# Kernel optimization log

Measured on AMD Instinct MI355X. Metric: run time of the kernel, lower is better.

The kernel has to match this reference:

```python
import jax, jax.numpy as jnp
import numpy as np

B, S = 65536, 128          # batch of tasks, support set size
MAX_CLASSES = 10
STATS_DIM = MAX_CLASSES + 4  # hist + [n_nonzero, entropy, subset_size, hist_max]
TOKEN_DIM = 256


def setup_inputs() -> dict:
    key = jax.random.key(0)
    k1, k2, k3, k4, k5 = jax.random.split(key, 5)
    y_support = jax.random.randint(k1, (B, S), 0, MAX_CLASSES, dtype=jnp.int32)
    # MLP params: Linear(14, D) -> GELU -> Linear(D, D)
    w1 = jax.random.normal(k2, (STATS_DIM, TOKEN_DIM), jnp.float32) / np.sqrt(STATS_DIM)
    b1 = jax.random.normal(k3, (TOKEN_DIM,), jnp.float32) * 0.01
    w2 = jax.random.normal(k4, (TOKEN_DIM, TOKEN_DIM), jnp.float32) / np.sqrt(TOKEN_DIM)
    b2 = jax.random.normal(k5, (TOKEN_DIM,), jnp.float32) * 0.01
    return {"y_support": y_support, "w1": w1, "b1": b1, "w2": w2, "b2": b2}


def reference(y_support, w1, b1, w2, b2):
    b, s = y_support.shape
    # Batched bincount via scatter-add: hist[i, c] = #{j : y_support[i, j] == c}
    rows = jnp.arange(b, dtype=jnp.int32)[:, None]              # [B, 1]
    hist = jnp.zeros((b, MAX_CLASSES), jnp.float32).at[rows, y_support].add(1.0)
    total = jnp.maximum(hist.sum(axis=-1, keepdims=True), 1.0)  # clamp_min(1.0)
    p = hist / total                                            # [B, C]
    entropy = -(p * jnp.log(p + 1e-6)).sum(axis=-1)             # [B]
    n_nonzero = (p > 0).sum(axis=-1).astype(jnp.float32)        # [B]
    stats = jnp.concatenate([
        p,
        n_nonzero[:, None],
        entropy[:, None],
        jnp.full((b, 1), float(s), jnp.float32),
        p.max(axis=-1, keepdims=True),
    ], axis=1)                                                  # [B, C+4]
    h = jax.nn.gelu(stats @ w1 + b1, approximate=False)         # exact GELU like nn.GELU
    return h @ w2 + b2                                          # [B, TOKEN_DIM]
```

## Files before the change

### kernel.cpp

```cpp
#include <hip/hip_runtime.h>
#include <stdint.h>


#define SSUP 128
#define DD   256

typedef __attribute__((ext_vector_type(8)))  short bf16x8;
typedef __attribute__((ext_vector_type(16))) float f32x16;

__device__ __forceinline__ unsigned f2bf_u(float f) {
    union { float f; unsigned u; } v; v.f = f;
    return (v.u + 0x7FFFu + ((v.u >> 16) & 1u)) >> 16;
}
__device__ __forceinline__ unsigned pk2(float a, float b) {
    return f2bf_u(a) | (f2bf_u(b) << 16);
}

__device__ __forceinline__ float gelu_f(float x) {
    float z = 0.7978845608028654f * x * (1.0f + 0.044715f * x * x);
    float e = __expf(-2.0f * z);
    float th = 2.0f / (1.0f + e) - 1.0f;
    return 0.5f * x * (1.0f + th);
}

__global__ void prep_kernel(const float* __restrict__ w1,
                            const float* __restrict__ w2,
                            unsigned short* __restrict__ w1f,
                            unsigned short* __restrict__ w2f) {
    int tid = blockIdx.x * 256 + threadIdx.x;
    if (tid < 8192) {
        int l  = tid & 63;
        int nt = (tid >> 6) & 7;
        int s  = tid >> 9;
        int n  = nt * 32 + (l & 31);
        int k0 = s * 16 + (l >> 5) * 8;
        unsigned pk[4];
        #pragma unroll
        for (int h = 0; h < 4; ++h)
            pk[h] = pk2(w2[(size_t)(k0 + 2*h) * DD + n],
                        w2[(size_t)(k0 + 2*h + 1) * DD + n]);
        *(uint4*)&w2f[(size_t)tid * 8] = make_uint4(pk[0], pk[1], pk[2], pk[3]);
    } else if (tid < 8704) {
        int idx = tid - 8192;
        int l   = idx & 63;
        int nt  = idx >> 6;
        int n   = nt * 32 + (l & 31);
        int kk0 = (l >> 5) * 8;
        unsigned pk[4];
        #pragma unroll
        for (int h = 0; h < 4; ++h) {
            int ka = kk0 + 2*h, kb = kk0 + 2*h + 1;
            float fa = (ka < 14) ? w1[(size_t)ka * DD + n] : 0.0f;
            float fb = (kb < 14) ? w1[(size_t)kb * DD + n] : 0.0f;
            pk[h] = pk2(fa, fb);
        }
        *(uint4*)&w1f[(size_t)idx * 8] = make_uint4(pk[0], pk[1], pk[2], pk[3]);
    }
}

__global__ __launch_bounds__(256, 4)
void encoder_kernel(const int* __restrict__ y,
                    const float* __restrict__ b1,
                    const float* __restrict__ b2,
                    const unsigned short* __restrict__ w1f,
                    const unsigned short* __restrict__ w2f,
                    float* __restrict__ out) {
    __shared__ __align__(16) unsigned short stats_a[64][16];
    __shared__ __align__(16) unsigned short h_lds[64][264];

    const int tid = threadIdx.x;
    const int r0 = blockIdx.x * 64;

    const int rl = tid >> 2;
    const int q  = tid & 3;
    const int4* yp = (const int4*)(y + (size_t)(r0 + rl) * SSUP);
    unsigned long long pkc = 0ull;
    #pragma unroll
    for (int i = 0; i < 8; ++i) {
        int4 v = yp[i * 4 + q];
        pkc += 1ull << (6 * v.x);
        pkc += 1ull << (6 * v.y);
        pkc += 1ull << (6 * v.z);
        pkc += 1ull << (6 * v.w);
    }
    float p[10]; float ent = 0.f, pmax = 0.f, nnz = 0.f;
    #pragma unroll
    for (int c = 0; c < 10; ++c) {
        int cc = (int)((pkc >> (6 * c)) & 63ull);
        cc += __shfl_xor(cc, 1);
        cc += __shfl_xor(cc, 2);
        float pc = (float)cc * 0.0078125f;
        p[c] = pc;
        nnz += (cc > 0) ? 1.0f : 0.0f;
        ent -= pc * __logf(pc + 1e-6f);
        pmax = fmaxf(pmax, pc);
    }
    if (q < 2) {
        unsigned a0, a1, a2, a3;
        if (q == 0) { a0 = pk2(p[0], p[1]); a1 = pk2(p[2], p[3]);
                      a2 = pk2(p[4], p[5]); a3 = pk2(p[6], p[7]); }
        else        { a0 = pk2(p[8], p[9]); a1 = pk2(nnz, ent);
                      a2 = pk2(128.0f, pmax); a3 = 0u; }
        *(uint4*)&stats_a[rl][q * 8] = make_uint4(a0, a1, a2, a3);
    }
    __syncthreads();

    const int lane = tid & 63;
    const int wid  = tid >> 6;
    const int wm   = wid & 1;
    const int wn   = wid >> 1;
    const int l31  = lane & 31;
    const int lh   = lane >> 5;

    bf16x8 af1 = *(const bf16x8*)&stats_a[32 * wm + l31][lh * 8];
    #pragma unroll
    for (int t = 0; t < 4; ++t) {
        const int nt  = wn * 4 + t;
        const int col = nt * 32 + l31;
        float bias = b1[col];
        f32x16 c;
        #pragma unroll
        for (int r = 0; r < 16; ++r) c[r] = bias;
        bf16x8 bf1 = *(const bf16x8*)&w1f[(size_t)(nt * 64 + lane) * 8];
        c = __builtin_amdgcn_mfma_f32_32x32x16_bf16(af1, bf1, c, 0, 0, 0);
        #pragma unroll
        for (int r = 0; r < 16; ++r) {
            int row = (r & 3) + 8 * (r >> 2) + 4 * lh;
            h_lds[32 * wm + row][col] = (unsigned short)f2bf_u(gelu_f(c[r]));
        }
    }
    __syncthreads();

    #pragma unroll
    for (int pass = 0; pass < 2; ++pass) {
        const int t0 = 2 * pass;
        f32x16 acc[2];
        #pragma unroll
        for (int u = 0; u < 2; ++u) {
            float bias = b2[(wn * 4 + t0 + u) * 32 + l31];
            #pragma unroll
            for (int r = 0; r < 16; ++r) acc[u][r] = bias;
        }
        #pragma unroll
        for (int s = 0; s < 16; ++s) {
            bf16x8 afr = *(const bf16x8*)&h_lds[32 * wm + l31][s * 16 + lh * 8];
            #pragma unroll
            for (int u = 0; u < 2; ++u) {
                const int nt = wn * 4 + t0 + u;
                bf16x8 bfr = *(const bf16x8*)
                    &w2f[(size_t)((s * 8 + nt) * 64 + lane) * 8];
                acc[u] = __builtin_amdgcn_mfma_f32_32x32x16_bf16(afr, bfr, acc[u], 0, 0, 0);
            }
        }
        #pragma unroll
        for (int u = 0; u < 2; ++u) {
            const int col = (wn * 4 + t0 + u) * 32 + l31;
            #pragma unroll
            for (int r = 0; r < 16; ++r) {
                int row = (r & 3) + 8 * (r >> 2) + 4 * lh;
                out[(size_t)(r0 + 32 * wm + row) * DD + col] = acc[u][r];
            }
        }
    }
}

extern "C" void kernel_launch(void* const* d_in, const int* in_sizes, int n_in,
                              void* d_out, int out_size, void* d_ws, size_t ws_size,
                              hipStream_t stream) {
    const int*   y  = (const int*)d_in[0];
    const float* w1 = (const float*)d_in[1];
    const float* b1 = (const float*)d_in[2];
    const float* w2 = (const float*)d_in[3];
    const float* b2 = (const float*)d_in[4];
    float* out = (float*)d_out;

    unsigned short* w2f = (unsigned short*)d_ws;
    unsigned short* w1f = w2f + 65536;

    prep_kernel<<<34, 256, 0, stream>>>(w1, w2, w1f, w2f);

    const int nrows = in_sizes[0] / SSUP;
    encoder_kernel<<<nrows / 64, 256, 0, stream>>>(y, b1, b2, w1f, w2f, out);
}
```

Before: 114.8 us.

## Swap MFMA operands for vectorized row stores and use 512-thread blocks

Swaps the MFMA operand order so each lane holds consecutive output columns of one row. This allows packed uint2 stores into LDS and float4 stores to global memory, where the old code did scattered scalar stores. The block grows to 512 threads (8 waves), so each wave computes fewer N tiles in a single pass, and the histogram load is spread over 8 threads per row with one extra shuffle. The larger block and stricter launch bounds could limit registers per thread.

```diff
diff --git a/kernel.cpp b/kernel.cpp
--- a/kernel.cpp
+++ b/kernel.cpp
@@ -58,7 +58,7 @@
     }
 }
 
-__global__ __launch_bounds__(256, 4)
+__global__ __launch_bounds__(512, 8)
 void encoder_kernel(const int* __restrict__ y,
                     const float* __restrict__ b1,
                     const float* __restrict__ b2,
@@ -71,13 +71,13 @@
     const int tid = threadIdx.x;
     const int r0 = blockIdx.x * 64;
 
-    const int rl = tid >> 2;
-    const int q  = tid & 3;
+    const int rl = tid >> 3;
+    const int q  = tid & 7;
     const int4* yp = (const int4*)(y + (size_t)(r0 + rl) * SSUP);
     unsigned long long pkc = 0ull;
     #pragma unroll
-    for (int i = 0; i < 8; ++i) {
-        int4 v = yp[i * 4 + q];
+    for (int i = 0; i < 4; ++i) {
+        int4 v = yp[i * 8 + q];
         pkc += 1ull << (6 * v.x);
         pkc += 1ull << (6 * v.y);
         pkc += 1ull << (6 * v.z);
@@ -89,6 +89,7 @@
         int cc = (int)((pkc >> (6 * c)) & 63ull);
         cc += __shfl_xor(cc, 1);
         cc += __shfl_xor(cc, 2);
+        cc += __shfl_xor(cc, 4);
         float pc = (float)cc * 0.0078125f;
         p[c] = pc;
         nnz += (cc > 0) ? 1.0f : 0.0f;
@@ -111,55 +112,60 @@
     const int wn   = wid >> 1;
     const int l31  = lane & 31;
     const int lh   = lane >> 5;
+    const int m    = 32 * wm + l31;
 
-    bf16x8 af1 = *(const bf16x8*)&stats_a[32 * wm + l31][lh * 8];
+    bf16x8 sfrag = *(const bf16x8*)&stats_a[m][lh * 8];
     #pragma unroll
-    for (int t = 0; t < 4; ++t) {
-        const int nt  = wn * 4 + t;
-        const int col = nt * 32 + l31;
-        float bias = b1[col];
+    for (int t = 0; t < 2; ++t) {
+        const int nt = wn * 2 + t;
+        bf16x8 wfrag = *(const bf16x8*)&w1f[(size_t)(nt * 64 + lane) * 8];
         f32x16 c;
         #pragma unroll
-        for (int r = 0; r < 16; ++r) c[r] = bias;
-        bf16x8 bf1 = *(const bf16x8*)&w1f[(size_t)(nt * 64 + lane) * 8];
-        c = __builtin_amdgcn_mfma_f32_32x32x16_bf16(af1, bf1, c, 0, 0, 0);
+        for (int g = 0; g < 4; ++g) {
+            float4 bv = *(const float4*)&b1[nt * 32 + 8 * g + 4 * lh];
+            c[4*g+0] = bv.x; c[4*g+1] = bv.y; c[4*g+2] = bv.z; c[4*g+3] = bv.w;
+        }
+        c = __builtin_amdgcn_mfma_f32_32x32x16_bf16(wfrag, sfrag, c, 0, 0, 0);
         #pragma unroll
-        for (int r = 0; r < 16; ++r) {
-            int row = (r & 3) + 8 * (r >> 2) + 4 * lh;
-            h_lds[32 * wm + row][col] = (unsigned short)f2bf_u(gelu_f(c[r]));
+        for (int g = 0; g < 4; ++g) {
+            unsigned u0 = pk2(gelu_f(c[4*g+0]), gelu_f(c[4*g+1]));
+            unsigned u1 = pk2(gelu_f(c[4*g+2]), gelu_f(c[4*g+3]));
+            *(uint2*)&h_lds[m][nt * 32 + 8 * g + 4 * lh] = make_uint2(u0, u1);
         }
     }
     __syncthreads();
 
+    f32x16 acc[2];
     #pragma unroll
-    for (int pass = 0; pass < 2; ++pass) {
-        const int t0 = 2 * pass;
-        f32x16 acc[2];
+    for (int u = 0; u < 2; ++u) {
+        const int nt = wn * 2 + u;
+        #pragma unroll
+        for (int g = 0; g < 4; ++g) {
+            float4 bv = *(const float4*)&b2[nt * 32 + 8 * g + 4 * lh];
+            acc[u][4*g+0] = bv.x; acc[u][4*g+1] = bv.y;
+            acc[u][4*g+2] = bv.z; acc[u][4*g+3] = bv.w;
+        }
+    }
+    #pragma unroll
+    for (int s = 0; s < 16; ++s) {
+        bf16x8 hfrag = *(const bf16x8*)&h_lds[m][s * 16 + lh * 8];
         #pragma unroll
         for (int u = 0; u < 2; ++u) {
-            float bias = b2[(wn * 4 + t0 + u) * 32 + l31];
-            #pragma unroll
-            for (int r = 0; r < 16; ++r) acc[u][r] = bias;
+            const int nt = wn * 2 + u;
+            bf16x8 wfrag = *(const bf16x8*)
+                &w2f[(size_t)((s * 8 + nt) * 64 + lane) * 8];
+            acc[u] = __builtin_amdgcn_mfma_f32_32x32x16_bf16(wfrag, hfrag, acc[u], 0, 0, 0);
         }
+    }
+    #pragma unroll
+    for (int u = 0; u < 2; ++u) {
+        const int nt = wn * 2 + u;
         #pragma unroll
-        for (int s = 0; s < 16; ++s) {
-            bf16x8 afr = *(const bf16x8*)&h_lds[32 * wm + l31][s * 16 + lh * 8];
-            #pragma unroll
-            for (int u = 0; u < 2; ++u) {
-                const int nt = wn * 4 + t0 + u;
-                bf16x8 bfr = *(const bf16x8*)
-                    &w2f[(size_t)((s * 8 + nt) * 64 + lane) * 8];
-                acc[u] = __builtin_amdgcn_mfma_f32_32x32x16_bf16(afr, bfr, acc[u], 0, 0, 0);
-            }
-        }
-        #pragma unroll
-        for (int u = 0; u < 2; ++u) {
-            const int col = (wn * 4 + t0 + u) * 32 + l31;
-            #pragma unroll
-            for (int r = 0; r < 16; ++r) {
-                int row = (r & 3) + 8 * (r >> 2) + 4 * lh;
-                out[(size_t)(r0 + 32 * wm + row) * DD + col] = acc[u][r];
-            }
+        for (int g = 0; g < 4; ++g) {
+            float4 o;
+            o.x = acc[u][4*g+0]; o.y = acc[u][4*g+1];
+            o.z = acc[u][4*g+2]; o.w = acc[u][4*g+3];
+            *(float4*)&out[(size_t)(r0 + m) * DD + nt * 32 + 8 * g + 4 * lh] = o;
         }
     }
 }
@@ -180,5 +186,5 @@
     prep_kernel<<<34, 256, 0, stream>>>(w1, w2, w1f, w2f);
 
     const int nrows = in_sizes[0] / SSUP;
-    encoder_kernel<<<nrows / 64, 256, 0, stream>>>(y, b1, b2, w1f, w2f, out);
+    encoder_kernel<<<nrows / 64, 512, 0, stream>>>(y, b1, b2, w1f, w2f, out);
 }
```

After: 120.7 us. 5.2% more time.
